# Kernel optimization log

Measured on AMD Instinct MI355X. Metric: run time of the kernel, lower is better.

The kernel has to match this reference:

```python
import jax, jax.numpy as jnp
import numpy as np

INFINITY = 1000000000000000.0


def setup_inputs() -> dict:
    key = jax.random.key(0)
    ks = jax.random.split(key, 6)
    B, Lq, Lk = 8, 256, 256
    Dq, Dk, A = 512, 512, 256
    Q = jax.random.normal(ks[0], (B, Lq, 1, Dq), dtype=jnp.float32)
    K = jax.random.normal(ks[1], (B, 1, Lk, Dk), dtype=jnp.float32)
    mask = jax.random.randint(ks[2], (B, Lq, Lk), 0, 2, dtype=jnp.int32)
    W1 = jax.random.normal(ks[3], (A, Dq), dtype=jnp.float32) / np.sqrt(Dq)
    W2 = jax.random.normal(ks[4], (A, Dk), dtype=jnp.float32) / np.sqrt(Dk)
    w3 = jax.random.normal(ks[5], (A,), dtype=jnp.float32) / np.sqrt(A)
    return {"Q": Q, "K": K, "mask": mask, "W1": W1, "W2": W2, "w3": w3}


def reference(Q, K, mask, W1, W2, w3):
    # Project then broadcast-add: [B,Lq,1,A] + [B,1,Lk,A] -> [B,Lq,Lk,A]
    q_proj = jnp.einsum('blqd,ad->blqa', Q, W1)  # [B,Lq,1,A]
    k_proj = jnp.einsum('bqkd,ad->bqka', K, W2)  # [B,1,Lk,A]
    score = jnp.einsum('blka,a->blk', jnp.tanh(q_proj + k_proj), w3)  # [B,Lq,Lk]
    score = jnp.where(mask == 0, -INFINITY, score)
    return jax.nn.softmax(score, axis=-1)
```

## Files before the change

### kernel.cpp

```cpp
#include <hip/hip_runtime.h>
#include <hip/hip_bf16.h>
#include <cstdint>

constexpr int B  = 8;
constexpr int LQ = 256;
constexpr int LK = 256;
constexpr int D  = 512;
constexpr int A  = 256;

constexpr float NEG_INF   = -1e15f;
constexpr float LOG2E     = 1.4426950408889634f;
constexpr float TWO_LOG2E = 2.8853900817779268f;

constexpr int QP_ELEMS = B * LQ * A;

constexpr int BM  = 64;
constexpr int BN  = 32;
constexpr int BKC = 64;
constexpr int LDK = 72;

typedef short bf16x8 __attribute__((ext_vector_type(8)));
typedef float f32x4  __attribute__((ext_vector_type(4)));

__device__ inline void split2(float x0, float x1, unsigned& hi, unsigned& lo) {
    unsigned u0 = __float_as_uint(x0), u1 = __float_as_uint(x1);
    unsigned h0 = u0 & 0xFFFF0000u, h1 = u1 & 0xFFFF0000u;
    hi = h1 | (u0 >> 16);
    float l0 = x0 - __uint_as_float(h0);
    float l1 = x1 - __uint_as_float(h1);
    lo = (__float_as_uint(l1) & 0xFFFF0000u) | (__float_as_uint(l0) >> 16);
}

__device__ inline void cvt8(float4 a, float4 b, uint4& hi, uint4& lo) {
    split2(a.x, a.y, hi.x, lo.x);
    split2(a.z, a.w, hi.y, lo.y);
    split2(b.x, b.y, hi.z, lo.z);
    split2(b.z, b.w, hi.w, lo.w);
}

__global__ __launch_bounds__(256) void proj_gemm(const float* __restrict__ Q,
                                                 const float* __restrict__ Kin,
                                                 const float* __restrict__ W1,
                                                 const float* __restrict__ W2,
                                                 float* __restrict__ qp,
                                                 float* __restrict__ kp) {
    __shared__ ushort AH[BM][LDK], AL[BM][LDK];
    __shared__ ushort BH[BN][LDK], BL[BN][LDK];

    const int t    = threadIdx.x;
    const int lane = t & 63;
    const int wave = t >> 6;
    const int wm   = (wave >> 1) * 32;
    const int wn   = (wave & 1) * 16;
    const int l15  = lane & 15;
    const int lg   = lane >> 4;

    const int tile_n  = blockIdx.x & 7;
    const int tile_m  = blockIdx.x >> 3;
    const int rowbase = tile_m * BM;
    const int cbase   = tile_n * BN;
    const bool isQ    = rowbase < 2048;

    const float* X  = isQ ? (Q + (size_t)rowbase * D)
                          : (Kin + (size_t)(rowbase - 2048) * D);
    const float* Wp = (isQ ? W1 : W2) + (size_t)cbase * D;

    const int sxm = t >> 2;
    const int sxk = (t & 3) * 16;
    const int swm = t >> 3;
    const int swk = (t & 7) * 8;

    const float* xrow = X + (size_t)sxm * D + sxk;
    const float* wrow = Wp + (size_t)swm * D + swk;

    f32x4 acc[2] = {{0.f, 0.f, 0.f, 0.f}, {0.f, 0.f, 0.f, 0.f}};

    for (int k0 = 0; k0 < D; k0 += BKC) {
        float4 xv0 = *(const float4*)(xrow + k0);
        float4 xv1 = *(const float4*)(xrow + k0 + 4);
        float4 xv2 = *(const float4*)(xrow + k0 + 8);
        float4 xv3 = *(const float4*)(xrow + k0 + 12);
        float4 wv0 = *(const float4*)(wrow + k0);
        float4 wv1 = *(const float4*)(wrow + k0 + 4);

        __syncthreads();

        uint4 h0, l0, h1, l1;
        cvt8(xv0, xv1, h0, l0);
        cvt8(xv2, xv3, h1, l1);
        *(uint4*)&AH[sxm][sxk]     = h0;
        *(uint4*)&AH[sxm][sxk + 8] = h1;
        *(uint4*)&AL[sxm][sxk]     = l0;
        *(uint4*)&AL[sxm][sxk + 8] = l1;

        uint4 hw, lw;
        cvt8(wv0, wv1, hw, lw);
        *(uint4*)&BH[swm][swk] = hw;
        *(uint4*)&BL[swm][swk] = lw;

        __syncthreads();

#pragma unroll
        for (int ks = 0; ks < BKC; ks += 32) {
            const int kf = ks + lg * 8;
            bf16x8 ah0 = *(const bf16x8*)&AH[wm + l15][kf];
            bf16x8 ah1 = *(const bf16x8*)&AH[wm + 16 + l15][kf];
            bf16x8 al0 = *(const bf16x8*)&AL[wm + l15][kf];
            bf16x8 al1 = *(const bf16x8*)&AL[wm + 16 + l15][kf];
            bf16x8 bh  = *(const bf16x8*)&BH[wn + l15][kf];
            bf16x8 bl  = *(const bf16x8*)&BL[wn + l15][kf];

            acc[0] = __builtin_amdgcn_mfma_f32_16x16x32_bf16(ah0, bh, acc[0], 0, 0, 0);
            acc[1] = __builtin_amdgcn_mfma_f32_16x16x32_bf16(ah1, bh, acc[1], 0, 0, 0);
            acc[0] = __builtin_amdgcn_mfma_f32_16x16x32_bf16(ah0, bl, acc[0], 0, 0, 0);
            acc[1] = __builtin_amdgcn_mfma_f32_16x16x32_bf16(ah1, bl, acc[1], 0, 0, 0);
            acc[0] = __builtin_amdgcn_mfma_f32_16x16x32_bf16(al0, bh, acc[0], 0, 0, 0);
            acc[1] = __builtin_amdgcn_mfma_f32_16x16x32_bf16(al1, bh, acc[1], 0, 0, 0);
        }
    }

    float ex[2][4];
#pragma unroll
    for (int mi = 0; mi < 2; ++mi)
#pragma unroll
        for (int r = 0; r < 4; ++r)
            ex[mi][r] = __builtin_amdgcn_exp2f(acc[mi][r] * TWO_LOG2E);

    if (isQ) {
#pragma unroll
        for (int mi = 0; mi < 2; ++mi)
#pragma unroll
            for (int r = 0; r < 4; ++r) {
                int row = rowbase + wm + mi * 16 + lg * 4 + r;
                int col = cbase + wn + l15;
                qp[(size_t)row * A + col] = ex[mi][r];
            }
    } else {
        __syncthreads();
        float* T = (float*)&AH[0][0];
#pragma unroll
        for (int mi = 0; mi < 2; ++mi)
#pragma unroll
            for (int r = 0; r < 4; ++r) {
                int m = wm + mi * 16 + lg * 4 + r;
                int n = wn + l15;
                T[m * 33 + n] = ex[mi][r];
            }
        __syncthreads();

        const int bb    = (rowbase - 2048) >> 8;
        const int kbase = rowbase & 255;
        float* dstb = kp + (size_t)bb * A * LK;
#pragma unroll
        for (int j = 0; j < 8; ++j) {
            int g  = j * 256 + t;
            int ii = g & 1;
            int kk = (g >> 1) & 63;
            int p  = g >> 7;
            dstb[((size_t)(tile_n * 16 + p) * LK + kbase + kk) * 2 + ii] =
                T[kk * 33 + 2 * p + ii];
        }
    }
}

__global__ __launch_bounds__(256) void score_softmax(const float* __restrict__ qp,
                                                     const float* __restrict__ kpT,
                                                     const int* __restrict__ mask,
                                                     const float* __restrict__ w3,
                                                     float* __restrict__ out) {
    const int t    = threadIdx.x;
    const int row0 = blockIdx.x * 4;
    const int b    = row0 >> 8;

    const float* kpb = kpT + (size_t)b * A * LK;
    const float* q0  = qp + (size_t)row0 * A;

    float acc0 = 0.f, acc1 = 0.f, acc2 = 0.f, acc3 = 0.f;

#pragma unroll 4
    for (int a = 0; a < A; a += 2) {
        float2 ek = *(const float2*)(kpb + ((size_t)(a >> 1) * LK + t) * 2);
        float w0  = w3[a], w1 = w3[a + 1];
        float q0a = q0[a],         q0b = q0[a + 1];
        float q1a = q0[A + a],     q1b = q0[A + a + 1];
        float q2a = q0[2 * A + a], q2b = q0[2 * A + a + 1];
        float q3a = q0[3 * A + a], q3b = q0[3 * A + a + 1];

        float f0 = 1.0f + q0a * ek.x;
        float f1 = 1.0f + q1a * ek.x;
        float f2 = 1.0f + q2a * ek.x;
        float f3 = 1.0f + q3a * ek.x;
        float rA = __builtin_amdgcn_rcpf(f0 * f1);
        float rB = __builtin_amdgcn_rcpf(f2 * f3);
        acc0 = fmaf(f1 * rA, w0, acc0);
        acc1 = fmaf(f0 * rA, w0, acc1);
        acc2 = fmaf(f3 * rB, w0, acc2);
        acc3 = fmaf(f2 * rB, w0, acc3);

        float g0 = 1.0f + q0b * ek.y;
        float g1 = 1.0f + q1b * ek.y;
        float g2 = 1.0f + q2b * ek.y;
        float g3 = 1.0f + q3b * ek.y;
        float rC = __builtin_amdgcn_rcpf(g0 * g1);
        float rD = __builtin_amdgcn_rcpf(g2 * g3);
        acc0 = fmaf(g1 * rC, w1, acc0);
        acc1 = fmaf(g0 * rC, w1, acc1);
        acc2 = fmaf(g3 * rD, w1, acc2);
        acc3 = fmaf(g2 * rD, w1, acc3);
    }

    const int* mrow = mask + (size_t)row0 * LK;
    float sc0 = (mrow[t]          == 0) ? NEG_INF : -2.0f * acc0;
    float sc1 = (mrow[LK + t]     == 0) ? NEG_INF : -2.0f * acc1;
    float sc2 = (mrow[2 * LK + t] == 0) ? NEG_INF : -2.0f * acc2;
    float sc3 = (mrow[3 * LK + t] == 0) ? NEG_INF : -2.0f * acc3;

    __shared__ float red[4][8];
    const int wave = t >> 6, lane = t & 63;

    float m0 = sc0, m1 = sc1, m2 = sc2, m3 = sc3;
#pragma unroll
    for (int off = 32; off > 0; off >>= 1) {
        m0 = fmaxf(m0, __shfl_xor(m0, off));
        m1 = fmaxf(m1, __shfl_xor(m1, off));
        m2 = fmaxf(m2, __shfl_xor(m2, off));
        m3 = fmaxf(m3, __shfl_xor(m3, off));
    }
    if (lane == 0) {
        red[0][wave] = m0; red[1][wave] = m1;
        red[2][wave] = m2; red[3][wave] = m3;
    }
    __syncthreads();
    float rmax0 = fmaxf(fmaxf(red[0][0], red[0][1]), fmaxf(red[0][2], red[0][3]));
    float rmax1 = fmaxf(fmaxf(red[1][0], red[1][1]), fmaxf(red[1][2], red[1][3]));
    float rmax2 = fmaxf(fmaxf(red[2][0], red[2][1]), fmaxf(red[2][2], red[2][3]));
    float rmax3 = fmaxf(fmaxf(red[3][0], red[3][1]), fmaxf(red[3][2], red[3][3]));
    __syncthreads();

    float p0 = __builtin_amdgcn_exp2f((sc0 - rmax0) * LOG2E);
    float p1 = __builtin_amdgcn_exp2f((sc1 - rmax1) * LOG2E);
    float p2 = __builtin_amdgcn_exp2f((sc2 - rmax2) * LOG2E);
    float p3 = __builtin_amdgcn_exp2f((sc3 - rmax3) * LOG2E);

    float s0 = p0, s1 = p1, s2 = p2, s3 = p3;
#pragma unroll
    for (int off = 32; off > 0; off >>= 1) {
        s0 += __shfl_xor(s0, off);
        s1 += __shfl_xor(s1, off);
        s2 += __shfl_xor(s2, off);
        s3 += __shfl_xor(s3, off);
    }
    if (lane == 0) {
        red[0][wave] = s0; red[1][wave] = s1;
        red[2][wave] = s2; red[3][wave] = s3;
    }
    __syncthreads();
    float sum0 = (red[0][0] + red[0][1]) + (red[0][2] + red[0][3]);
    float sum1 = (red[1][0] + red[1][1]) + (red[1][2] + red[1][3]);
    float sum2 = (red[2][0] + red[2][1]) + (red[2][2] + red[2][3]);
    float sum3 = (red[3][0] + red[3][1]) + (red[3][2] + red[3][3]);

    out[(size_t)row0 * LK + t]       = p0 * __builtin_amdgcn_rcpf(sum0);
    out[(size_t)(row0 + 1) * LK + t] = p1 * __builtin_amdgcn_rcpf(sum1);
    out[(size_t)(row0 + 2) * LK + t] = p2 * __builtin_amdgcn_rcpf(sum2);
    out[(size_t)(row0 + 3) * LK + t] = p3 * __builtin_amdgcn_rcpf(sum3);
}

extern "C" void kernel_launch(void* const* d_in, const int* in_sizes, int n_in,
                              void* d_out, int out_size, void* d_ws, size_t ws_size,
                              hipStream_t stream) {
    const float* Q    = (const float*)d_in[0];
    const float* K    = (const float*)d_in[1];
    const int*   mask = (const int*)d_in[2];
    const float* W1   = (const float*)d_in[3];
    const float* W2   = (const float*)d_in[4];
    const float* w3   = (const float*)d_in[5];
    float* out = (float*)d_out;

    float* ws  = (float*)d_ws;
    float* qp  = ws;
    float* kpT = ws + QP_ELEMS;

    proj_gemm<<<512, 256, 0, stream>>>(Q, K, W1, W2, qp, kpT);
    score_softmax<<<(B * LQ) / 4, 256, 0, stream>>>(qp, kpT, mask, w3, out);
}
```

Measured before the change: 39.28 us.

## Halve projection GEMM M-tile, switch key layout to quads, simplify score loop

The projection GEMM tile shrinks from 64 to 32 rows, so each wave owns one 16x16 output and the grid doubles to 1024 blocks, giving more blocks per GPU and less work per block. The transposed key projection is now stored in groups of four along the attention dimension, so the score kernel can read it with float4 loads. The score loop drops the shared-reciprocal pairing trick and issues one reciprocal per element, which cuts multiplies but doubles transcendental instructions. The smaller GEMM tile also means operand data is reused less per block.

```diff
diff --git a/kernel.cpp b/kernel.cpp
--- a/kernel.cpp
+++ b/kernel.cpp
@@ -14,7 +14,7 @@
 
 constexpr int QP_ELEMS = B * LQ * A;
 
-constexpr int BM  = 64;
+constexpr int BM  = 32;
 constexpr int BN  = 32;
 constexpr int BKC = 64;
 constexpr int LDK = 72;
@@ -50,7 +50,7 @@
     const int t    = threadIdx.x;
     const int lane = t & 63;
     const int wave = t >> 6;
-    const int wm   = (wave >> 1) * 32;
+    const int wm   = (wave >> 1) * 16;
     const int wn   = (wave & 1) * 16;
     const int l15  = lane & 15;
     const int lg   = lane >> 4;
@@ -65,100 +65,80 @@
                           : (Kin + (size_t)(rowbase - 2048) * D);
     const float* Wp = (isQ ? W1 : W2) + (size_t)cbase * D;
 
-    const int sxm = t >> 2;
-    const int sxk = (t & 3) * 16;
-    const int swm = t >> 3;
-    const int swk = (t & 7) * 8;
-
-    const float* xrow = X + (size_t)sxm * D + sxk;
-    const float* wrow = Wp + (size_t)swm * D + swk;
-
-    f32x4 acc[2] = {{0.f, 0.f, 0.f, 0.f}, {0.f, 0.f, 0.f, 0.f}};
+    const int sm = t >> 3;
+    const int sk = (t & 7) * 8;
+
+    const float* xrow = X + (size_t)sm * D + sk;
+    const float* wrow = Wp + (size_t)sm * D + sk;
+
+    f32x4 acc = {0.f, 0.f, 0.f, 0.f};
 
     for (int k0 = 0; k0 < D; k0 += BKC) {
         float4 xv0 = *(const float4*)(xrow + k0);
         float4 xv1 = *(const float4*)(xrow + k0 + 4);
-        float4 xv2 = *(const float4*)(xrow + k0 + 8);
-        float4 xv3 = *(const float4*)(xrow + k0 + 12);
         float4 wv0 = *(const float4*)(wrow + k0);
         float4 wv1 = *(const float4*)(wrow + k0 + 4);
 
         __syncthreads();
 
-        uint4 h0, l0, h1, l1;
-        cvt8(xv0, xv1, h0, l0);
-        cvt8(xv2, xv3, h1, l1);
-        *(uint4*)&AH[sxm][sxk]     = h0;
-        *(uint4*)&AH[sxm][sxk + 8] = h1;
-        *(uint4*)&AL[sxm][sxk]     = l0;
-        *(uint4*)&AL[sxm][sxk + 8] = l1;
-
-        uint4 hw, lw;
+        uint4 hx, lx, hw, lw;
+        cvt8(xv0, xv1, hx, lx);
         cvt8(wv0, wv1, hw, lw);
-        *(uint4*)&BH[swm][swk] = hw;
-        *(uint4*)&BL[swm][swk] = lw;
+        *(uint4*)&AH[sm][sk] = hx;
+        *(uint4*)&AL[sm][sk] = lx;
+        *(uint4*)&BH[sm][sk] = hw;
+        *(uint4*)&BL[sm][sk] = lw;
 
         __syncthreads();
 
 #pragma unroll
         for (int ks = 0; ks < BKC; ks += 32) {
             const int kf = ks + lg * 8;
-            bf16x8 ah0 = *(const bf16x8*)&AH[wm + l15][kf];
-            bf16x8 ah1 = *(const bf16x8*)&AH[wm + 16 + l15][kf];
-            bf16x8 al0 = *(const bf16x8*)&AL[wm + l15][kf];
-            bf16x8 al1 = *(const bf16x8*)&AL[wm + 16 + l15][kf];
-            bf16x8 bh  = *(const bf16x8*)&BH[wn + l15][kf];
-            bf16x8 bl  = *(const bf16x8*)&BL[wn + l15][kf];
-
-            acc[0] = __builtin_amdgcn_mfma_f32_16x16x32_bf16(ah0, bh, acc[0], 0, 0, 0);
-            acc[1] = __builtin_amdgcn_mfma_f32_16x16x32_bf16(ah1, bh, acc[1], 0, 0, 0);
-            acc[0] = __builtin_amdgcn_mfma_f32_16x16x32_bf16(ah0, bl, acc[0], 0, 0, 0);
-            acc[1] = __builtin_amdgcn_mfma_f32_16x16x32_bf16(ah1, bl, acc[1], 0, 0, 0);
-            acc[0] = __builtin_amdgcn_mfma_f32_16x16x32_bf16(al0, bh, acc[0], 0, 0, 0);
-            acc[1] = __builtin_amdgcn_mfma_f32_16x16x32_bf16(al1, bh, acc[1], 0, 0, 0);
-        }
-    }
-
-    float ex[2][4];
-#pragma unroll
-    for (int mi = 0; mi < 2; ++mi)
-#pragma unroll
-        for (int r = 0; r < 4; ++r)
-            ex[mi][r] = __builtin_amdgcn_exp2f(acc[mi][r] * TWO_LOG2E);
+            bf16x8 ah = *(const bf16x8*)&AH[wm + l15][kf];
+            bf16x8 al = *(const bf16x8*)&AL[wm + l15][kf];
+            bf16x8 bh = *(const bf16x8*)&BH[wn + l15][kf];
+            bf16x8 bl = *(const bf16x8*)&BL[wn + l15][kf];
+
+            acc = __builtin_amdgcn_mfma_f32_16x16x32_bf16(ah, bh, acc, 0, 0, 0);
+            acc = __builtin_amdgcn_mfma_f32_16x16x32_bf16(ah, bl, acc, 0, 0, 0);
+            acc = __builtin_amdgcn_mfma_f32_16x16x32_bf16(al, bh, acc, 0, 0, 0);
+        }
+    }
+
+    float ex[4];
+#pragma unroll
+    for (int r = 0; r < 4; ++r)
+        ex[r] = __builtin_amdgcn_exp2f(acc[r] * TWO_LOG2E);
 
     if (isQ) {
 #pragma unroll
-        for (int mi = 0; mi < 2; ++mi)
-#pragma unroll
-            for (int r = 0; r < 4; ++r) {
-                int row = rowbase + wm + mi * 16 + lg * 4 + r;
-                int col = cbase + wn + l15;
-                qp[(size_t)row * A + col] = ex[mi][r];
-            }
+        for (int r = 0; r < 4; ++r) {
+            int row = rowbase + wm + lg * 4 + r;
+            int col = cbase + wn + l15;
+            qp[(size_t)row * A + col] = ex[r];
+        }
     } else {
         __syncthreads();
         float* T = (float*)&AH[0][0];
 #pragma unroll
-        for (int mi = 0; mi < 2; ++mi)
-#pragma unroll
-            for (int r = 0; r < 4; ++r) {
-                int m = wm + mi * 16 + lg * 4 + r;
-                int n = wn + l15;
-                T[m * 33 + n] = ex[mi][r];
-            }
+        for (int r = 0; r < 4; ++r) {
+            int m = wm + lg * 4 + r;
+            int n = wn + l15;
+            T[m * 33 + n] = ex[r];
+        }
         __syncthreads();
 
         const int bb    = (rowbase - 2048) >> 8;
         const int kbase = rowbase & 255;
         float* dstb = kp + (size_t)bb * A * LK;
 #pragma unroll
-        for (int j = 0; j < 8; ++j) {
+        for (int j = 0; j < 4; ++j) {
             int g  = j * 256 + t;
-            int ii = g & 1;
-            int kk = (g >> 1) & 63;
+            int ii = g & 3;
+            int kk = (g >> 2) & 31;
             int p  = g >> 7;
-            dstb[((size_t)(tile_n * 16 + p) * LK + kbase + kk) * 2 + ii] =
-                T[kk * 33 + 2 * p + ii];
+            dstb[((size_t)(tile_n * 8 + p) * LK + kbase + kk) * 4 + ii] =
+                T[kk * 33 + 4 * p + ii];
         }
     }
 }
@@ -175,45 +155,28 @@
     const float* kpb = kpT + (size_t)b * A * LK;
     const float* q0  = qp + (size_t)row0 * A;
 
-    float acc0 = 0.f, acc1 = 0.f, acc2 = 0.f, acc3 = 0.f;
+    float acc[4] = {0.f, 0.f, 0.f, 0.f};
 
 #pragma unroll 4
-    for (int a = 0; a < A; a += 2) {
-        float2 ek = *(const float2*)(kpb + ((size_t)(a >> 1) * LK + t) * 2);
-        float w0  = w3[a], w1 = w3[a + 1];
-        float q0a = q0[a],         q0b = q0[a + 1];
-        float q1a = q0[A + a],     q1b = q0[A + a + 1];
-        float q2a = q0[2 * A + a], q2b = q0[2 * A + a + 1];
-        float q3a = q0[3 * A + a], q3b = q0[3 * A + a + 1];
-
-        float f0 = 1.0f + q0a * ek.x;
-        float f1 = 1.0f + q1a * ek.x;
-        float f2 = 1.0f + q2a * ek.x;
-        float f3 = 1.0f + q3a * ek.x;
-        float rA = __builtin_amdgcn_rcpf(f0 * f1);
-        float rB = __builtin_amdgcn_rcpf(f2 * f3);
-        acc0 = fmaf(f1 * rA, w0, acc0);
-        acc1 = fmaf(f0 * rA, w0, acc1);
-        acc2 = fmaf(f3 * rB, w0, acc2);
-        acc3 = fmaf(f2 * rB, w0, acc3);
-
-        float g0 = 1.0f + q0b * ek.y;
-        float g1 = 1.0f + q1b * ek.y;
-        float g2 = 1.0f + q2b * ek.y;
-        float g3 = 1.0f + q3b * ek.y;
-        float rC = __builtin_amdgcn_rcpf(g0 * g1);
-        float rD = __builtin_amdgcn_rcpf(g2 * g3);
-        acc0 = fmaf(g1 * rC, w1, acc0);
-        acc1 = fmaf(g0 * rC, w1, acc1);
-        acc2 = fmaf(g3 * rD, w1, acc2);
-        acc3 = fmaf(g2 * rD, w1, acc3);
+    for (int a = 0; a < A; a += 4) {
+        float4 ekv = *(const float4*)(kpb + ((size_t)(a >> 2) * LK + t) * 4);
+        float ek[4] = {ekv.x, ekv.y, ekv.z, ekv.w};
+#pragma unroll
+        for (int j = 0; j < 4; ++j) {
+            float w = w3[a + j];
+#pragma unroll
+            for (int r = 0; r < 4; ++r) {
+                float f = fmaf(q0[r * A + a + j], ek[j], 1.0f);
+                acc[r] = fmaf(__builtin_amdgcn_rcpf(f), w, acc[r]);
+            }
+        }
     }
 
     const int* mrow = mask + (size_t)row0 * LK;
-    float sc0 = (mrow[t]          == 0) ? NEG_INF : -2.0f * acc0;
-    float sc1 = (mrow[LK + t]     == 0) ? NEG_INF : -2.0f * acc1;
-    float sc2 = (mrow[2 * LK + t] == 0) ? NEG_INF : -2.0f * acc2;
-    float sc3 = (mrow[3 * LK + t] == 0) ? NEG_INF : -2.0f * acc3;
+    float sc0 = (mrow[t]          == 0) ? NEG_INF : -2.0f * acc[0];
+    float sc1 = (mrow[LK + t]     == 0) ? NEG_INF : -2.0f * acc[1];
+    float sc2 = (mrow[2 * LK + t] == 0) ? NEG_INF : -2.0f * acc[2];
+    float sc3 = (mrow[3 * LK + t] == 0) ? NEG_INF : -2.0f * acc[3];
 
     __shared__ float red[4][8];
     const int wave = t >> 6, lane = t & 63;
@@ -281,6 +244,6 @@
     float* qp  = ws;
     float* kpT = ws + QP_ELEMS;
 
-    proj_gemm<<<512, 256, 0, stream>>>(Q, K, W1, W2, qp, kpT);
+    proj_gemm<<<1024, 256, 0, stream>>>(Q, K, W1, W2, qp, kpT);
     score_softmax<<<(B * LQ) / 4, 256, 0, stream>>>(qp, kpT, mask, w3, out);
 }
```

New measurement: 42.58 us. 1.08x slower.

## Pre-split inputs to bf16 hi/lo in separate pass before projection GEMM

Applied to the files above, without the earlier changes.

Adds a split_pass kernel that converts Q, K, W1 and W2 into bf16 hi/lo pairs in workspace once, so the projection GEMM loads ready-made bf16 tiles instead of converting fp32 on every tile load. The intent is to stop redundant conversion of the weights, which each block repeats, and to cut ALU work in the GEMM loop. In exchange it adds a kernel launch plus an extra global write and read of about 4.6M bf16 values. It also raises the unroll of the score loop from 4 to 8.

```diff
diff --git a/kernel.cpp b/kernel.cpp
--- a/kernel.cpp
+++ b/kernel.cpp
@@ -13,6 +13,8 @@
 constexpr float TWO_LOG2E = 2.8853900817779268f;
 
 constexpr int QP_ELEMS = B * LQ * A;
+constexpr int XROWS    = 4096;
+constexpr int WROWS    = 512;
 
 constexpr int BM  = 64;
 constexpr int BN  = 32;
@@ -38,10 +40,45 @@
     split2(b.z, b.w, hi.w, lo.w);
 }
 
-__global__ __launch_bounds__(256) void proj_gemm(const float* __restrict__ Q,
-                                                 const float* __restrict__ Kin,
-                                                 const float* __restrict__ W1,
-                                                 const float* __restrict__ W2,
+__global__ __launch_bounds__(256) void split_pass(const float* __restrict__ Q,
+                                                  const float* __restrict__ Kin,
+                                                  const float* __restrict__ W1,
+                                                  const float* __restrict__ W2,
+                                                  ushort* __restrict__ XH,
+                                                  ushort* __restrict__ XL,
+                                                  ushort* __restrict__ WH,
+                                                  ushort* __restrict__ WL) {
+    const int XTH = (XROWS * D) / 8;
+    int g = blockIdx.x * 256 + threadIdx.x;
+    if (g < XTH) {
+        int base = g * 8;
+        int row = base >> 9, k = base & 511;
+        const float* src = (row < 2048) ? (Q + (size_t)row * D + k)
+                                        : (Kin + (size_t)(row - 2048) * D + k);
+        float4 a = *(const float4*)src;
+        float4 b = *(const float4*)(src + 4);
+        uint4 h, l;
+        cvt8(a, b, h, l);
+        *(uint4*)&XH[base] = h;
+        *(uint4*)&XL[base] = l;
+    } else {
+        int base = (g - XTH) * 8;
+        int row = base >> 9, k = base & 511;
+        const float* src = (row < 256) ? (W1 + (size_t)row * D + k)
+                                       : (W2 + (size_t)(row - 256) * D + k);
+        float4 a = *(const float4*)src;
+        float4 b = *(const float4*)(src + 4);
+        uint4 h, l;
+        cvt8(a, b, h, l);
+        *(uint4*)&WH[base] = h;
+        *(uint4*)&WL[base] = l;
+    }
+}
+
+__global__ __launch_bounds__(256) void proj_gemm(const ushort* __restrict__ XH,
+                                                 const ushort* __restrict__ XL,
+                                                 const ushort* __restrict__ WH,
+                                                 const ushort* __restrict__ WL,
                                                  float* __restrict__ qp,
                                                  float* __restrict__ kp) {
     __shared__ ushort AH[BM][LDK], AL[BM][LDK];
@@ -61,42 +98,35 @@
     const int cbase   = tile_n * BN;
     const bool isQ    = rowbase < 2048;
 
-    const float* X  = isQ ? (Q + (size_t)rowbase * D)
-                          : (Kin + (size_t)(rowbase - 2048) * D);
-    const float* Wp = (isQ ? W1 : W2) + (size_t)cbase * D;
-
     const int sxm = t >> 2;
     const int sxk = (t & 3) * 16;
     const int swm = t >> 3;
     const int swk = (t & 7) * 8;
 
-    const float* xrow = X + (size_t)sxm * D + sxk;
-    const float* wrow = Wp + (size_t)swm * D + swk;
+    const ushort* xh = XH + (size_t)(rowbase + sxm) * D;
+    const ushort* xl = XL + (size_t)(rowbase + sxm) * D;
+    const int wrow = (isQ ? 0 : 256) + cbase + swm;
+    const ushort* wh = WH + (size_t)wrow * D;
+    const ushort* wl = WL + (size_t)wrow * D;
 
     f32x4 acc[2] = {{0.f, 0.f, 0.f, 0.f}, {0.f, 0.f, 0.f, 0.f}};
 
     for (int k0 = 0; k0 < D; k0 += BKC) {
-        float4 xv0 = *(const float4*)(xrow + k0);
-        float4 xv1 = *(const float4*)(xrow + k0 + 4);
-        float4 xv2 = *(const float4*)(xrow + k0 + 8);
-        float4 xv3 = *(const float4*)(xrow + k0 + 12);
-        float4 wv0 = *(const float4*)(wrow + k0);
-        float4 wv1 = *(const float4*)(wrow + k0 + 4);
+        uint4 vxh0 = *(const uint4*)&xh[k0 + sxk];
+        uint4 vxh1 = *(const uint4*)&xh[k0 + sxk + 8];
+        uint4 vxl0 = *(const uint4*)&xl[k0 + sxk];
+        uint4 vxl1 = *(const uint4*)&xl[k0 + sxk + 8];
+        uint4 vwh  = *(const uint4*)&wh[k0 + swk];
+        uint4 vwl  = *(const uint4*)&wl[k0 + swk];
 
         __syncthreads();
 
-        uint4 h0, l0, h1, l1;
-        cvt8(xv0, xv1, h0, l0);
-        cvt8(xv2, xv3, h1, l1);
-        *(uint4*)&AH[sxm][sxk]     = h0;
-        *(uint4*)&AH[sxm][sxk + 8] = h1;
-        *(uint4*)&AL[sxm][sxk]     = l0;
-        *(uint4*)&AL[sxm][sxk + 8] = l1;
-
-        uint4 hw, lw;
-        cvt8(wv0, wv1, hw, lw);
-        *(uint4*)&BH[swm][swk] = hw;
-        *(uint4*)&BL[swm][swk] = lw;
+        *(uint4*)&AH[sxm][sxk]     = vxh0;
+        *(uint4*)&AH[sxm][sxk + 8] = vxh1;
+        *(uint4*)&AL[sxm][sxk]     = vxl0;
+        *(uint4*)&AL[sxm][sxk + 8] = vxl1;
+        *(uint4*)&BH[swm][swk]     = vwh;
+        *(uint4*)&BL[swm][swk]     = vwl;
 
         __syncthreads();
 
@@ -177,7 +207,7 @@
 
     float acc0 = 0.f, acc1 = 0.f, acc2 = 0.f, acc3 = 0.f;
 
-#pragma unroll 4
+#pragma unroll 8
     for (int a = 0; a < A; a += 2) {
         float2 ek = *(const float2*)(kpb + ((size_t)(a >> 1) * LK + t) * 2);
         float w0  = w3[a], w1 = w3[a + 1];
@@ -278,9 +308,16 @@
     float* out = (float*)d_out;
 
     float* ws  = (float*)d_ws;
-    float* qp  = ws;
-    float* kpT = ws + QP_ELEMS;
-
-    proj_gemm<<<512, 256, 0, stream>>>(Q, K, W1, W2, qp, kpT);
+    float*  qp  = ws;
+    float*  kpT = ws + QP_ELEMS;
+    ushort* XH  = (ushort*)(ws + 2 * QP_ELEMS);
+    ushort* XL  = XH + (size_t)XROWS * D;
+    ushort* WH  = XL + (size_t)XROWS * D;
+    ushort* WL  = WH + (size_t)WROWS * D;
+
+    const int xblocks = (XROWS * D) / 8 / 256;
+    const int wblocks = (WROWS * D) / 8 / 256;
+    split_pass<<<xblocks + wblocks, 256, 0, stream>>>(Q, K, W1, W2, XH, XL, WH, WL);
+    proj_gemm<<<512, 256, 0, stream>>>(XH, XL, WH, WL, qp, kpT);
     score_softmax<<<(B * LQ) / 4, 256, 0, stream>>>(qp, kpT, mask, w3, out);
 }
```

Measured after the change: 46.16 us. 1.18x slower.
